# Kernel optimization log

Measured on AMD Instinct MI355X. Metric: run time of the kernel, lower is better.

## Reference

```python
import jax, jax.numpy as jnp
import numpy as np

NUM_GRAPHS = 128
EPS = 1e-5


def _instance_norm(x, seg):
    # per-graph (segment) normalization over rows, per channel; affine=False (PyG default)
    ones = jnp.ones((x.shape[0],), x.dtype)
    cnt = jnp.maximum(jax.ops.segment_sum(ones, seg, num_segments=NUM_GRAPHS), 1.0)[:, None]
    mean = jax.ops.segment_sum(x, seg, num_segments=NUM_GRAPHS) / cnt
    ex2 = jax.ops.segment_sum(x * x, seg, num_segments=NUM_GRAPHS) / cnt
    var = jnp.maximum(ex2 - mean * mean, 0.0)
    return (x - mean[seg]) * jax.lax.rsqrt(var[seg] + EPS)


def setup_inputs() -> dict:
    key = jax.random.key(0)
    ks = jax.random.split(key, 6)
    N, E, H = 100_000, 1_600_000, 64
    emb = jax.random.normal(ks[0], (N, H), jnp.float32)
    edge_index = jax.random.randint(ks[1], (2, E), 0, N)
    batch = jnp.sort(jax.random.randint(ks[2], (N,), 0, NUM_GRAPHS))
    s = lambda fan: 1.0 / np.sqrt(fan)
    # MLP layers [2H, 4H, H, 1]
    W1 = jax.random.uniform(ks[3], (2 * H, 4 * H), jnp.float32, -s(2 * H), s(2 * H))
    b1 = jnp.zeros((4 * H,), jnp.float32)
    W2 = jax.random.uniform(ks[4], (4 * H, H), jnp.float32, -s(4 * H), s(4 * H))
    b2 = jnp.zeros((H,), jnp.float32)
    W3 = jax.random.uniform(ks[5], (H, 1), jnp.float32, -s(H), s(H))
    b3 = jnp.zeros((1,), jnp.float32)
    return dict(emb=emb, edge_index=edge_index, batch=batch,
                W1=W1, b1=b1, W2=W2, b2=b2, W3=W3, b3=b3)


def reference(emb, edge_index, batch, W1, b1, W2, b2, W3, b3):
    col, row = edge_index[0], edge_index[1]
    # edge-wise gather + concat: [E, 2H]
    f12 = jnp.concatenate([emb[col], emb[row]], axis=-1)
    seg = batch[col]  # graph id per edge
    h = jax.nn.relu(_instance_norm(f12 @ W1 + b1, seg))   # [E, 4H]
    h = jax.nn.relu(_instance_norm(h @ W2 + b2, seg))     # [E, H]
    att_log_logits = h @ W3 + b3                          # [E, 1]
    return att_log_logits
```

## Files before the change

kernel.cpp:

```cpp
#include <hip/hip_runtime.h>
#include <hip/hip_bf16.h>

#define NSEG 128
#define H64 64
#define C1 256
#define K1 128
#define C2 64
#define EPSV 1e-5f
#define NWG 256

typedef __attribute__((ext_vector_type(8))) short bf16x8;
typedef __attribute__((ext_vector_type(16))) float f32x16;
typedef __attribute__((ext_vector_type(4))) unsigned int u32x4;

struct BTrue  { static constexpr bool value = true; };
struct BFalse { static constexpr bool value = false; };

__device__ __forceinline__ unsigned short f2bf(float f){
  unsigned int x = __float_as_uint(f);
  x += 0x7fffu + ((x >> 16) & 1u);
  return (unsigned short)(x >> 16);
}
__device__ __forceinline__ float bf2f(unsigned short u){
  return __uint_as_float(((unsigned int)u) << 16);
}
__device__ __forceinline__ unsigned pkbf(float lo, float hi){
  unsigned r;
  asm("v_cvt_pk_bf16_f32 %0, %1, %2" : "=v"(r) : "v"(lo), "v"(hi));
  return r;
}
__device__ __forceinline__ bf16x8 mk8(unsigned a, unsigned b, unsigned c, unsigned d){
  u32x4 t = {a, b, c, d};
  return __builtin_bit_cast(bf16x8, t);
}
__device__ __forceinline__ int xcd_swz(int bid, int nwg){
  int q = nwg >> 3, r = nwg & 7;
  int x = bid & 7, o = bid >> 3;
  return (x < r ? x * (q + 1) : r * (q + 1) + (x - r) * q) + o;
}

__global__ void k_cvt_emb(const float* __restrict__ src, unsigned short* __restrict__ dst, int n4){
  int i = blockIdx.x * blockDim.x + threadIdx.x;
  if (i >= n4) return;
  float4 v = ((const float4*)src)[i];
  unsigned int a = (unsigned int)f2bf(v.x) | ((unsigned int)f2bf(v.y) << 16);
  unsigned int b = (unsigned int)f2bf(v.z) | ((unsigned int)f2bf(v.w) << 16);
  ((uint2*)dst)[i] = make_uint2(a, b);
}

__global__ void k_cvt_w(const float* __restrict__ W1, const float* __restrict__ W2,
                        unsigned short* __restrict__ W1T, unsigned short* __restrict__ W2T){
  int i = blockIdx.x * blockDim.x + threadIdx.x;
  if (i < C1 * K1){
    int c = i >> 7, k = i & 127;
    W1T[i] = f2bf(W1[k * C1 + c]);
  } else {
    int j = i - C1 * K1;
    if (j < C2 * C1){
      int c = j >> 8, k = j & 255;
      W2T[j] = f2bf(W2[k * C2 + c]);
    }
  }
}

__global__ void k_hist(const int* __restrict__ col, const int* __restrict__ batch,
                       int* __restrict__ segE, int* __restrict__ cnt, int E){
  __shared__ int h[NSEG];
  for (int i = threadIdx.x; i < NSEG; i += blockDim.x) h[i] = 0;
  __syncthreads();
  int stride = gridDim.x * blockDim.x;
  for (int e = blockIdx.x * blockDim.x + threadIdx.x; e < E; e += stride){
    int s = batch[col[e]];
    segE[e] = s;
    atomicAdd(&h[s], 1);
  }
  __syncthreads();
  for (int i = threadIdx.x; i < NSEG; i += blockDim.x)
    if (h[i]) atomicAdd(&cnt[i], h[i]);
}

__global__ void k_scan(const int* __restrict__ cnt, int* __restrict__ cursor,
                       float* __restrict__ cntf){
  if (threadIdx.x == 0){
    int acc = 0;
    for (int i = 0; i < NSEG; i++){ cursor[i] = acc; acc += cnt[i]; }
  }
  if (threadIdx.x < NSEG){
    int c = cnt[threadIdx.x];
    cntf[threadIdx.x] = (float)(c > 0 ? c : 1);
  }
}

__global__ void k_scatter(const int* __restrict__ segE, const int* __restrict__ ei,
                          int* __restrict__ cursor, int* __restrict__ perm,
                          int* __restrict__ segS, int* __restrict__ ecol, int* __restrict__ erow,
                          int E, int epb){
  __shared__ int h[NSEG];
  __shared__ int base[NSEG];
  int b0 = blockIdx.x * epb;
  int b1 = b0 + epb < E ? b0 + epb : E;
  for (int i = threadIdx.x; i < NSEG; i += blockDim.x) h[i] = 0;
  __syncthreads();
  for (int e = b0 + threadIdx.x; e < b1; e += blockDim.x) atomicAdd(&h[segE[e]], 1);
  __syncthreads();
  for (int i = threadIdx.x; i < NSEG; i += blockDim.x)
    base[i] = h[i] ? atomicAdd(&cursor[i], h[i]) : 0;
  __syncthreads();
  for (int i = threadIdx.x; i < NSEG; i += blockDim.x) h[i] = 0;
  __syncthreads();
  for (int e = b0 + threadIdx.x; e < b1; e += blockDim.x){
    int s = segE[e];
    int p = base[s] + atomicAdd(&h[s], 1);
    perm[p] = e; segS[p] = s;
    ecol[p] = ei[e]; erow[p] = ei[(size_t)E + e];
  }
}

__global__ void __launch_bounds__(1024, 4)
k_stats1(const unsigned short* __restrict__ ebf, const unsigned short* __restrict__ W1T,
         const int* __restrict__ ecol, const int* __restrict__ erow, const int* __restrict__ segS,
         float* __restrict__ sum1, float* __restrict__ sq1, int NWT, int E, int T)
{
  __shared__ __align__(16) char wl[65536];
  {
    #pragma unroll
    for (int j = 0; j < 4; j++){
      int i = threadIdx.x + j * 1024;
      int r = i >> 4, u = i & 15;
      u32x4 v = *(const u32x4*)(W1T + (size_t)r * K1 + u * 8);
      *(u32x4*)(wl + r * 256 + ((u ^ (r & 15)) << 4)) = v;
    }
  }
  __syncthreads();

  const int lane = threadIdx.x & 63, w = threadIdx.x >> 6;
  const int g = lane >> 5, l31 = lane & 31;
  const int bid = xcd_swz(blockIdx.x, NWG);
  const int wt0 = (bid * 16 + w) * T;
  float psum[8] = {0,0,0,0,0,0,0,0}, psq[8] = {0,0,0,0,0,0,0,0};
  int cur = -1;

  auto flush = [&](int seg){
    if (seg < 0) return;
    #pragma unroll
    for (int nt = 0; nt < 8; nt++){
      float sv = psum[nt] + __shfl_xor(psum[nt], 32);
      float qv = psq[nt]  + __shfl_xor(psq[nt], 32);
      if (lane < 32){
        atomicAdd(&sum1[seg * C1 + nt * 32 + l31], sv);
        atomicAdd(&sq1 [seg * C1 + nt * 32 + l31], qv);
      }
      psum[nt] = 0.f; psq[nt] = 0.f;
    }
  };

  for (int it = 0; it < T; ++it){
    int wt = wt0 + it;
    if (wt >= NWT) break;
    const int p0 = wt * 32;
    int e0 = p0 + l31;
    int e0c = e0 < E ? e0 : E - 1;
    int cA = ecol[e0c], rA = erow[e0c];
    int sg = segS[e0c];

    bf16x8 fa[8];
    #pragma unroll
    for (int kk = 0; kk < 8; kk++){
      int off = (kk & 3) * 16 + g * 8;
      fa[kk] = *(const bf16x8*)(ebf + (size_t)(kk < 4 ? cA : rA) * H64 + off);
    }

    int sA = __builtin_amdgcn_readfirstlane(__shfl(sg, 0));
    int sB = __builtin_amdgcn_readfirstlane(__shfl(sg, 31));
    bool uni = (sA == sB) && (p0 + 32 <= E);
    if (uni && sA != cur){ flush(cur); cur = sA; }
    if (!uni){ flush(cur); cur = -1; }

    #pragma unroll 1
    for (int nt = 0; nt < 8; nt++){
      f32x16 a0;
      #pragma unroll
      for (int r = 0; r < 16; r++) a0[r] = 0.f;
      const int rw = nt * 32 + l31;
      __builtin_amdgcn_s_setprio(1);
      #pragma unroll
      for (int kk = 0; kk < 8; kk++){
        bf16x8 b = *(const bf16x8*)(wl + rw * 256 + (((2 * kk + g) ^ (rw & 15)) << 4));
        a0 = __builtin_amdgcn_mfma_f32_32x32x16_bf16(fa[kk], b, a0, 0, 0, 0);
      }
      __builtin_amdgcn_s_setprio(0);
      if (uni){
        float ts = 0.f, tq = 0.f;
        #pragma unroll
        for (int r = 0; r < 16; r++){ ts += a0[r]; tq += a0[r] * a0[r]; }
        psum[nt] += ts; psq[nt] += tq;
      } else {
        for (int s = sA; s <= sB; s++){
          float ts = 0.f, tq = 0.f;
          #pragma unroll
          for (int r = 0; r < 16; r++){
            int c = (r & 3) + 8 * (r >> 2) + 4 * g;
            bool ok = (__shfl(sg, c) == s) && (p0 + c < E);
            float v = ok ? a0[r] : 0.f;
            ts += v; tq += v * v;
          }
          float sv = ts + __shfl_xor(ts, 32);
          float qv = tq + __shfl_xor(tq, 32);
          if (lane < 32){
            atomicAdd(&sum1[s * C1 + nt * 32 + l31], sv);
            atomicAdd(&sq1 [s * C1 + nt * 32 + l31], qv);
          }
        }
      }
    }
  }
  flush(cur);
}

__global__ void k_fin(const float* __restrict__ sum, const float* __restrict__ sq,
                      const float* __restrict__ cntf,
                      float* __restrict__ sc, float* __restrict__ sh, int C){
  int i = blockIdx.x * blockDim.x + threadIdx.x;
  if (i >= NSEG * C) return;
  int s = i / C;
  float c = cntf[s];
  float m = sum[i] / c;
  float v = fmaxf(sq[i] / c - m * m, 0.f);
  float inv = rsqrtf(v + EPSV);
  sc[i] = inv;
  sh[i] = -m * inv;
}

template<int MODE>
__global__ void __launch_bounds__(1024, 4)
k_mid(const unsigned short* __restrict__ ebf, const unsigned short* __restrict__ W1T,
      const unsigned short* __restrict__ W2T,
      const int* __restrict__ ecol, const int* __restrict__ erow,
      const int* __restrict__ segS, const int* __restrict__ perm,
      const float* __restrict__ sc1, const float* __restrict__ sh1,
      float* __restrict__ sum2, float* __restrict__ sq2,
      unsigned int* __restrict__ y2u,
      const float* __restrict__ sc2, const float* __restrict__ sh2,
      const float* __restrict__ W3, const float* __restrict__ b3,
      float* __restrict__ out, int NWT, int E, int T)
{
  __shared__ __align__(16) char wl[98304];
  {
    #pragma unroll
    for (int j = 0; j < 4; j++){
      int i = threadIdx.x + j * 1024;
      int r = i >> 4, u = i & 15;
      u32x4 v = *(const u32x4*)(W1T + (size_t)r * K1 + u * 8);
      *(u32x4*)(wl + r * 256 + ((u ^ (r & 15)) << 4)) = v;
    }
    #pragma unroll
    for (int j = 0; j < 2; j++){
      int i = threadIdx.x + j * 1024;
      int r = i >> 5, u = i & 31;
      u32x4 v = *(const u32x4*)(W2T + (size_t)r * C1 + u * 8);
      *(u32x4*)(wl + 65536 + r * 512 + ((u ^ (r & 31)) << 4)) = v;
    }
  }
  __syncthreads();

  const int lane = threadIdx.x & 63, w = threadIdx.x >> 6;
  const int g = lane >> 5, l31 = lane & 31;
  const int bid = xcd_swz(blockIdx.x, NWG);
  const int wt0 = (bid * 16 + w) * T;

  float b3v = 0.f;
  if (MODE == 2) b3v = b3[0];

  auto body = [&](auto uni_c, const bf16x8* fbp, int sgn, int sAr, f32x16* acc2){
    constexpr bool UNI = decltype(uni_c)::value;
    #pragma unroll 1
    for (int mt = 0; mt < 8; mt++){
      f32x16 a1;
      #pragma unroll
      for (int r = 0; r < 16; r++) a1[r] = 0.f;
      const int rw = mt * 32 + l31;
      __builtin_amdgcn_s_setprio(1);
      #pragma unroll
      for (int kk = 0; kk < 8; kk++){
        bf16x8 wa = *(const bf16x8*)(wl + rw * 256 + (((2 * kk + g) ^ (rw & 15)) << 4));
        a1 = __builtin_amdgcn_mfma_f32_32x32x16_bf16(wa, fbp[kk], a1, 0, 0, 0);
      }
      __builtin_amdgcn_s_setprio(0);
      const float* scp; const float* shp;
      if constexpr (UNI){
        scp = sc1 + sAr * C1 + mt * 32;
        shp = sh1 + sAr * C1 + mt * 32;
      } else {
        scp = sc1 + sgn * C1 + mt * 32;
        shp = sh1 + sgn * C1 + mt * 32;
      }
      unsigned pk_[8];
      #pragma unroll
      for (int rq = 0; rq < 4; rq++){
        float4 sc = *(const float4*)(scp + rq * 8 + 4 * g);
        float4 sh = *(const float4*)(shp + rq * 8 + 4 * g);
        float h0 = fmaxf(fmaf(a1[rq * 4 + 0], sc.x, sh.x), 0.f);
        float h1 = fmaxf(fmaf(a1[rq * 4 + 1], sc.y, sh.y), 0.f);
        float h2 = fmaxf(fmaf(a1[rq * 4 + 2], sc.z, sh.z), 0.f);
        float h3 = fmaxf(fmaf(a1[rq * 4 + 3], sc.w, sh.w), 0.f);
        pk_[rq * 2 + 0] = pkbf(h0, h1);
        pk_[rq * 2 + 1] = pkbf(h2, h3);
      }
      asm("v_permlane32_swap_b32 %0, %1" : "+v"(pk_[0]), "+v"(pk_[2]));
      asm("v_permlane32_swap_b32 %0, %1" : "+v"(pk_[1]), "+v"(pk_[3]));
      asm("v_permlane32_swap_b32 %0, %1" : "+v"(pk_[4]), "+v"(pk_[6]));
      asm("v_permlane32_swap_b32 %0, %1" : "+v"(pk_[5]), "+v"(pk_[7]));
      bf16x8 bf0 = mk8(pk_[0], pk_[1], pk_[2], pk_[3]);
      bf16x8 bf1 = mk8(pk_[4], pk_[5], pk_[6], pk_[7]);
      __builtin_amdgcn_s_setprio(1);
      #pragma unroll
      for (int ct = 0; ct < 2; ct++){
        int rb = ct * 32 + l31;
        bf16x8 wb0 = *(const bf16x8*)(wl + 65536 + rb * 512 + (((4 * mt + g) ^ (rb & 31)) << 4));
        bf16x8 wb1 = *(const bf16x8*)(wl + 65536 + rb * 512 + (((4 * mt + 2 + g) ^ (rb & 31)) << 4));
        acc2[ct] = __builtin_amdgcn_mfma_f32_32x32x16_bf16(wb0, bf0, acc2[ct], 0, 0, 0);
        acc2[ct] = __builtin_amdgcn_mfma_f32_32x32x16_bf16(wb1, bf1, acc2[ct], 0, 0, 0);
      }
      __builtin_amdgcn_s_setprio(0);
    }
  };

  for (int it = 0; it < T; ++it){
    int wt = wt0 + it;
    if (wt >= NWT) break;
    const int p0 = wt * 32;
    int e0 = p0 + l31;
    bool v0 = e0 < E;
    int e0c = v0 ? e0 : E - 1;
    int cA = ecol[e0c], rA = erow[e0c];
    int sg = segS[e0c];

    bf16x8 fb[8];
    #pragma unroll
    for (int kk = 0; kk < 8; kk++){
      int off = (kk & 3) * 16 + g * 8;
      fb[kk] = *(const bf16x8*)(ebf + (size_t)(kk < 4 ? cA : rA) * H64 + off);
    }

    int sA = __builtin_amdgcn_readfirstlane(__shfl(sg, 0));
    int sB = __builtin_amdgcn_readfirstlane(__shfl(sg, 31));
    const bool uni = (sA == sB) && (p0 + 32 <= E);

    f32x16 acc2[2];
    #pragma unroll
    for (int ct = 0; ct < 2; ct++)
      #pragma unroll
      for (int r = 0; r < 16; r++) acc2[ct][r] = 0.f;

    if (uni) body(BTrue{},  fb, sg, sA, acc2);
    else     body(BFalse{}, fb, sg, sA, acc2);

    if constexpr (MODE == 0){
      if (v0){
        unsigned* yp = y2u + (size_t)e0 * 32;
        #pragma unroll
        for (int ct = 0; ct < 2; ct++)
          #pragma unroll
          for (int rq = 0; rq < 4; rq++){
            uint2 pv;
            pv.x = pkbf(acc2[ct][rq * 4 + 0], acc2[ct][rq * 4 + 1]);
            pv.y = pkbf(acc2[ct][rq * 4 + 2], acc2[ct][rq * 4 + 3]);
            *(uint2*)(yp + ct * 16 + rq * 4 + 2 * g) = pv;
          }
      }
    } else if constexpr (MODE == 1){
      for (int s = sA; s <= sB; s++){
        #pragma unroll
        for (int ct = 0; ct < 2; ct++)
          #pragma unroll
          for (int r = 0; r < 16; r++){
            float x = (v0 && sg == s) ? acc2[ct][r] : 0.f;
            float vs = x, vq = x * x;
            #pragma unroll
            for (int off = 1; off < 32; off <<= 1){
              vs += __shfl_xor(vs, off);
              vq += __shfl_xor(vq, off);
            }
            if (l31 == 0){
              int c2 = ct * 32 + (r & 3) + 8 * (r >> 2) + 4 * g;
              atomicAdd(&sum2[s * C2 + c2], vs);
              atomicAdd(&sq2 [s * C2 + c2], vq);
            }
          }
      }
    } else {
      float acc = 0.f;
      #pragma unroll
      for (int ct = 0; ct < 2; ct++)
        #pragma unroll
        for (int rq = 0; rq < 4; rq++){
          float4 sc = *(const float4*)(sc2 + sg * C2 + ct * 32 + rq * 8 + 4 * g);
          float4 sh = *(const float4*)(sh2 + sg * C2 + ct * 32 + rq * 8 + 4 * g);
          float4 wq = *(const float4*)(W3 + ct * 32 + rq * 8 + 4 * g);
          acc = fmaf(fmaxf(fmaf(acc2[ct][rq * 4 + 0], sc.x, sh.x), 0.f), wq.x, acc);
          acc = fmaf(fmaxf(fmaf(acc2[ct][rq * 4 + 1], sc.y, sh.y), 0.f), wq.y, acc);
          acc = fmaf(fmaxf(fmaf(acc2[ct][rq * 4 + 2], sc.z, sh.z), 0.f), wq.z, acc);
          acc = fmaf(fmaxf(fmaf(acc2[ct][rq * 4 + 3], sc.w, sh.w), 0.f), wq.w, acc);
        }
      acc += __shfl_xor(acc, 32);
      if (g == 0 && v0) out[perm[e0]] = acc + b3v;
    }
  }
}

__global__ void k_stats2(const unsigned int* __restrict__ y2u, const int* __restrict__ segS,
                         float* __restrict__ sum2, float* __restrict__ sq2, int E)
{
  const int cp = threadIdx.x & 31;
  const int es = threadIdx.x >> 5;
  int chunk = (E + gridDim.x - 1) / gridDim.x;
  int eb = blockIdx.x * chunk;
  int ee = eb + chunk < E ? eb + chunk : E;
  float s0 = 0.f, s1 = 0.f, q0 = 0.f, q1 = 0.f;
  int cur = -1;
  for (int e = eb + es; e < ee; e += 8){
    int sg = segS[e];
    unsigned v = y2u[(size_t)e * 32 + cp];
    float f0 = bf2f((unsigned short)(v & 0xffff));
    float f1 = bf2f((unsigned short)(v >> 16));
    if (sg != cur){
      if (cur >= 0){
        atomicAdd(&sum2[cur * C2 + 2 * cp], s0);
        atomicAdd(&sum2[cur * C2 + 2 * cp + 1], s1);
        atomicAdd(&sq2 [cur * C2 + 2 * cp], q0);
        atomicAdd(&sq2 [cur * C2 + 2 * cp + 1], q1);
      }
      s0 = s1 = q0 = q1 = 0.f; cur = sg;
    }
    s0 += f0; s1 += f1; q0 += f0 * f0; q1 += f1 * f1;
  }
  if (cur >= 0){
    atomicAdd(&sum2[cur * C2 + 2 * cp], s0);
    atomicAdd(&sum2[cur * C2 + 2 * cp + 1], s1);
    atomicAdd(&sq2 [cur * C2 + 2 * cp], q0);
    atomicAdd(&sq2 [cur * C2 + 2 * cp + 1], q1);
  }
}

__global__ void k_out(const unsigned short* __restrict__ y2, const int* __restrict__ segS,
                      const int* __restrict__ perm, const float* __restrict__ sc2,
                      const float* __restrict__ sh2, const float* __restrict__ W3,
                      const float* __restrict__ b3, float* __restrict__ out, int E)
{
  const int lane = threadIdx.x & 63;
  const int wid = (blockIdx.x * blockDim.x + threadIdx.x) >> 6;
  const int nw = (gridDim.x * blockDim.x) >> 6;
  const int es = lane >> 3;
  const int cp = (lane & 7) * 8;
  float w3r[8];
  #pragma unroll
  for (int j = 0; j < 8; j++) w3r[j] = W3[cp + j];
  const float b3v = b3[0];
  for (long base = (long)wid * 8; base < E; base += (long)nw * 8){
    int pos = (int)base + es;
    float a = 0.f;
    if (pos < E){
      bf16x8 v = *(const bf16x8*)(y2 + (size_t)pos * C2 + cp);
      int s = segS[pos];
      const float* scp = sc2 + s * C2 + cp;
      const float* shp = sh2 + s * C2 + cp;
      #pragma unroll
      for (int j = 0; j < 8; j++){
        float hv = fmaxf(fmaf(bf2f((unsigned short)v[j]), scp[j], shp[j]), 0.f);
        a = fmaf(hv, w3r[j], a);
      }
    }
    a += __shfl_xor(a, 1); a += __shfl_xor(a, 2); a += __shfl_xor(a, 4);
    if ((lane & 7) == 0 && pos < E) out[perm[pos]] = a + b3v;
  }
}

extern "C" void kernel_launch(void* const* d_in, const int* in_sizes, int n_in,
                              void* d_out, int out_size, void* d_ws, size_t ws_size,
                              hipStream_t stream)
{
  const float* emb   = (const float*)d_in[0];
  const int*   ei    = (const int*)d_in[1];
  const int*   batch = (const int*)d_in[2];
  const float* W1    = (const float*)d_in[3];
  const float* W2    = (const float*)d_in[5];
  const float* W3    = (const float*)d_in[7];
  const float* b3    = (const float*)d_in[8];
  float* out = (float*)d_out;
  const int E = in_sizes[1] / 2;
  const int N = in_sizes[0] / H64;
  const int NWT = (E + 31) / 32;

  char* ws = (char*)d_ws;
  size_t o = 0;
  auto al = [&](size_t b){ size_t r = o; o = (o + b + 255) & ~((size_t)255); return r; };
  size_t o_ebf  = al((size_t)N * H64 * 2);
  size_t o_w1t  = al((size_t)C1 * K1 * 2);
  size_t o_w2t  = al((size_t)C2 * C1 * 2);
  size_t o_perm = al((size_t)E * 4);
  size_t o_segS = al((size_t)E * 4);
  size_t o_ecol = al((size_t)E * 4);
  size_t o_erow = al((size_t)E * 4);
  size_t o_cnt  = al(NSEG * 4);
  size_t o_cur  = al(NSEG * 4);
  size_t o_cntf = al(NSEG * 4);
  size_t o_sum1 = al((size_t)NSEG * C1 * 4);
  size_t o_sq1  = al((size_t)NSEG * C1 * 4);
  size_t o_sum2 = al((size_t)NSEG * C2 * 4);
  size_t o_sq2  = al((size_t)NSEG * C2 * 4);
  size_t o_sc1  = al((size_t)NSEG * C1 * 4);
  size_t o_sh1  = al((size_t)NSEG * C1 * 4);
  size_t o_sc2  = al((size_t)NSEG * C2 * 4);
  size_t o_sh2  = al((size_t)NSEG * C2 * 4);
  size_t o_segE = al((size_t)E * 4);
  size_t o_y2   = o_segE;
  size_t need_full = o_segE + (size_t)E * C2 * 2;
  const bool full = ws_size >= need_full;

  unsigned short* ebf = (unsigned short*)(ws + o_ebf);
  unsigned short* W1T = (unsigned short*)(ws + o_w1t);
  unsigned short* W2T = (unsigned short*)(ws + o_w2t);
  int* perm = (int*)(ws + o_perm);
  int* segS = (int*)(ws + o_segS);
  int* ecol = (int*)(ws + o_ecol);
  int* erow = (int*)(ws + o_erow);
  int* cnt  = (int*)(ws + o_cnt);
  int* curp = (int*)(ws + o_cur);
  float* cntf = (float*)(ws + o_cntf);
  float* sum1 = (float*)(ws + o_sum1);
  float* sq1  = (float*)(ws + o_sq1);
  float* sum2 = (float*)(ws + o_sum2);
  float* sq2  = (float*)(ws + o_sq2);
  float* sc1  = (float*)(ws + o_sc1);
  float* sh1  = (float*)(ws + o_sh1);
  float* sc2  = (float*)(ws + o_sc2);
  float* sh2  = (float*)(ws + o_sh2);
  int* segE = (int*)(ws + o_segE);
  unsigned int* y2u = (unsigned int*)(ws + o_y2);
  unsigned short* y2 = (unsigned short*)(ws + o_y2);

  hipMemsetAsync(ws + o_cnt, 0, o_sc1 - o_cnt, stream);

  k_cvt_emb<<<(N * H64 / 4 + 255) / 256, 256, 0, stream>>>(emb, ebf, N * H64 / 4);
  k_cvt_w<<<192, 256, 0, stream>>>(W1, W2, W1T, W2T);

  k_hist<<<2048, 256, 0, stream>>>(ei, batch, segE, cnt, E);
  k_scan<<<1, 128, 0, stream>>>(cnt, curp, cntf);
  const int epb = 2048;
  k_scatter<<<(E + epb - 1) / epb, 256, 0, stream>>>(segE, ei, curp, perm, segS, ecol, erow, E, epb);

  const int T = (NWT + NWG * 16 - 1) / (NWG * 16);
  k_stats1<<<NWG, 1024, 0, stream>>>(ebf, W1T, ecol, erow, segS, sum1, sq1, NWT, E, T);
  k_fin<<<(NSEG * C1) / 256, 256, 0, stream>>>(sum1, sq1, cntf, sc1, sh1, C1);

  if (full){
    k_mid<0><<<NWG, 1024, 0, stream>>>(ebf, W1T, W2T, ecol, erow, segS, perm,
        sc1, sh1, sum2, sq2, y2u, sc2, sh2, W3, b3, out, NWT, E, T);
    k_stats2<<<512, 256, 0, stream>>>(y2u, segS, sum2, sq2, E);
    k_fin<<<(NSEG * C2) / 256, 256, 0, stream>>>(sum2, sq2, cntf, sc2, sh2, C2);
    k_out<<<1024, 256, 0, stream>>>(y2, segS, perm, sc2, sh2, W3, b3, out, E);
  } else {
    k_mid<1><<<NWG, 1024, 0, stream>>>(ebf, W1T, W2T, ecol, erow, segS, perm,
        sc1, sh1, sum2, sq2, nullptr, sc2, sh2, W3, b3, out, NWT, E, T);
    k_fin<<<(NSEG * C2) / 256, 256, 0, stream>>>(sum2, sq2, cntf, sc2, sh2, C2);
    k_mid<2><<<NWG, 1024, 0, stream>>>(ebf, W1T, W2T, ecol, erow, segS, perm,
        sc1, sh1, sum2, sq2, nullptr, sc2, sh2, W3, b3, out, NWT, E, T);
  }
}
```

Baseline: 700.9 us.

## Prefetch next tile indices, pair MFMA tiles, cache norm params in LDS

Edge indices and segment ids for the next 32-edge tile are loaded one iteration ahead, so their latency is hidden behind the current tile's MFMA work. In the stats1 kernel two output column tiles are now computed per loop iteration, which gives the MFMA pipe two independent accumulator chains. In k_mid the per-segment scale and shift vectors are staged into a per-wave LDS slot when the segment changes, replacing repeated global reads on the uniform path. The cost is extra registers, which could lower occupancy under the 1024x4 launch bounds, plus another 32KB of shared memory on top of 96KB that may limit the number of resident blocks.

```diff
diff --git a/kernel.cpp b/kernel.cpp
--- a/kernel.cpp
+++ b/kernel.cpp
@@ -154,14 +154,22 @@
     }
   };
 
+  auto ld3 = [&](int wt, int& a, int& r, int& s){
+    int e = wt * 32 + l31;
+    int ec = e < E ? e : E - 1;
+    a = ecol[ec]; r = erow[ec]; s = segS[ec];
+  };
+
+  int cA, rA, sg;
+  if (wt0 < NWT) ld3(wt0, cA, rA, sg);
+
   for (int it = 0; it < T; ++it){
     int wt = wt0 + it;
     if (wt >= NWT) break;
     const int p0 = wt * 32;
-    int e0 = p0 + l31;
-    int e0c = e0 < E ? e0 : E - 1;
-    int cA = ecol[e0c], rA = erow[e0c];
-    int sg = segS[e0c];
+    int nA, nR, nS;
+    const bool hv = (it + 1 < T) && (wt + 1 < NWT);
+    if (hv) ld3(wt + 1, nA, nR, nS);
 
     bf16x8 fa[8];
     #pragma unroll
@@ -177,42 +185,56 @@
     if (!uni){ flush(cur); cur = -1; }
 
     #pragma unroll 1
-    for (int nt = 0; nt < 8; nt++){
-      f32x16 a0;
-      #pragma unroll
-      for (int r = 0; r < 16; r++) a0[r] = 0.f;
-      const int rw = nt * 32 + l31;
+    for (int np = 0; np < 4; np++){
+      const int nt0 = 2 * np, nt1 = 2 * np + 1;
+      f32x16 a0, a1;
+      #pragma unroll
+      for (int r = 0; r < 16; r++){ a0[r] = 0.f; a1[r] = 0.f; }
+      const int rw0 = nt0 * 32 + l31, rw1 = nt1 * 32 + l31;
       __builtin_amdgcn_s_setprio(1);
       #pragma unroll
       for (int kk = 0; kk < 8; kk++){
-        bf16x8 b = *(const bf16x8*)(wl + rw * 256 + (((2 * kk + g) ^ (rw & 15)) << 4));
-        a0 = __builtin_amdgcn_mfma_f32_32x32x16_bf16(fa[kk], b, a0, 0, 0, 0);
+        bf16x8 b0 = *(const bf16x8*)(wl + rw0 * 256 + (((2 * kk + g) ^ (rw0 & 15)) << 4));
+        bf16x8 b1 = *(const bf16x8*)(wl + rw1 * 256 + (((2 * kk + g) ^ (rw1 & 15)) << 4));
+        a0 = __builtin_amdgcn_mfma_f32_32x32x16_bf16(fa[kk], b0, a0, 0, 0, 0);
+        a1 = __builtin_amdgcn_mfma_f32_32x32x16_bf16(fa[kk], b1, a1, 0, 0, 0);
       }
       __builtin_amdgcn_s_setprio(0);
       if (uni){
-        float ts = 0.f, tq = 0.f;
+        float t0 = 0.f, q0 = 0.f, t1 = 0.f, q1 = 0.f;
         #pragma unroll
-        for (int r = 0; r < 16; r++){ ts += a0[r]; tq += a0[r] * a0[r]; }
-        psum[nt] += ts; psq[nt] += tq;
+        for (int r = 0; r < 16; r++){
+          t0 += a0[r]; q0 += a0[r] * a0[r];
+          t1 += a1[r]; q1 += a1[r] * a1[r];
+        }
+        psum[nt0] += t0; psq[nt0] += q0;
+        psum[nt1] += t1; psq[nt1] += q1;
       } else {
         for (int s = sA; s <= sB; s++){
-          float ts = 0.f, tq = 0.f;
+          float t0 = 0.f, q0 = 0.f, t1 = 0.f, q1 = 0.f;
           #pragma unroll
           for (int r = 0; r < 16; r++){
             int c = (r & 3) + 8 * (r >> 2) + 4 * g;
             bool ok = (__shfl(sg, c) == s) && (p0 + c < E);
-            float v = ok ? a0[r] : 0.f;
-            ts += v; tq += v * v;
+            float v0 = ok ? a0[r] : 0.f;
+            float v1 = ok ? a1[r] : 0.f;
+            t0 += v0; q0 += v0 * v0;
+            t1 += v1; q1 += v1 * v1;
           }
-          float sv = ts + __shfl_xor(ts, 32);
-          float qv = tq + __shfl_xor(tq, 32);
+          float s0 = t0 + __shfl_xor(t0, 32);
+          float qq0 = q0 + __shfl_xor(q0, 32);
+          float s1 = t1 + __shfl_xor(t1, 32);
+          float qq1 = q1 + __shfl_xor(q1, 32);
           if (lane < 32){
-            atomicAdd(&sum1[s * C1 + nt * 32 + l31], sv);
-            atomicAdd(&sq1 [s * C1 + nt * 32 + l31], qv);
+            atomicAdd(&sum1[s * C1 + nt0 * 32 + l31], s0);
+            atomicAdd(&sq1 [s * C1 + nt0 * 32 + l31], qq0);
+            atomicAdd(&sum1[s * C1 + nt1 * 32 + l31], s1);
+            atomicAdd(&sq1 [s * C1 + nt1 * 32 + l31], qq1);
           }
         }
       }
     }
+    if (hv){ cA = nA; rA = nR; sg = nS; }
   }
   flush(cur);
 }
@@ -245,6 +267,7 @@
       float* __restrict__ out, int NWT, int E, int T)
 {
   __shared__ __align__(16) char wl[98304];
+  __shared__ __align__(16) float scsh[16][512];
   {
     #pragma unroll
     for (int j = 0; j < 4; j++){
@@ -270,8 +293,9 @@
 
   float b3v = 0.f;
   if (MODE == 2) b3v = b3[0];
-
-  auto body = [&](auto uni_c, const bf16x8* fbp, int sgn, int sAr, f32x16* acc2){
+  int wseg = -1;
+
+  auto body = [&](auto uni_c, const bf16x8* fbp, int sgn, f32x16* acc2){
     constexpr bool UNI = decltype(uni_c)::value;
     #pragma unroll 1
     for (int mt = 0; mt < 8; mt++){
@@ -286,19 +310,17 @@
         a1 = __builtin_amdgcn_mfma_f32_32x32x16_bf16(wa, fbp[kk], a1, 0, 0, 0);
       }
       __builtin_amdgcn_s_setprio(0);
-      const float* scp; const float* shp;
-      if constexpr (UNI){
-        scp = sc1 + sAr * C1 + mt * 32;
-        shp = sh1 + sAr * C1 + mt * 32;
-      } else {
-        scp = sc1 + sgn * C1 + mt * 32;
-        shp = sh1 + sgn * C1 + mt * 32;
-      }
       unsigned pk_[8];
       #pragma unroll
       for (int rq = 0; rq < 4; rq++){
-        float4 sc = *(const float4*)(scp + rq * 8 + 4 * g);
-        float4 sh = *(const float4*)(shp + rq * 8 + 4 * g);
+        float4 sc, sh;
+        if constexpr (UNI){
+          sc = *(const float4*)(&scsh[w][mt * 32 + rq * 8 + 4 * g]);
+          sh = *(const float4*)(&scsh[w][256 + mt * 32 + rq * 8 + 4 * g]);
+        } else {
+          sc = *(const float4*)(sc1 + sgn * C1 + mt * 32 + rq * 8 + 4 * g);
+          sh = *(const float4*)(sh1 + sgn * C1 + mt * 32 + rq * 8 + 4 * g);
+        }
         float h0 = fmaxf(fmaf(a1[rq * 4 + 0], sc.x, sh.x), 0.f);
         float h1 = fmaxf(fmaf(a1[rq * 4 + 1], sc.y, sh.y), 0.f);
         float h2 = fmaxf(fmaf(a1[rq * 4 + 2], sc.z, sh.z), 0.f);
@@ -325,15 +347,25 @@
     }
   };
 
+  auto ld3 = [&](int wt, int& a, int& r, int& s){
+    int e = wt * 32 + l31;
+    int ec = e < E ? e : E - 1;
+    a = ecol[ec]; r = erow[ec]; s = segS[ec];
+  };
+
+  int cA, rA, sg;
+  if (wt0 < NWT) ld3(wt0, cA, rA, sg);
+
   for (int it = 0; it < T; ++it){
     int wt = wt0 + it;
     if (wt >= NWT) break;
     const int p0 = wt * 32;
+    int nA, nR, nS;
+    const bool hv = (it + 1 < T) && (wt + 1 < NWT);
+    if (hv) ld3(wt + 1, nA, nR, nS);
+
     int e0 = p0 + l31;
     bool v0 = e0 < E;
-    int e0c = v0 ? e0 : E - 1;
-    int cA = ecol[e0c], rA = erow[e0c];
-    int sg = segS[e0c];
 
     bf16x8 fb[8];
     #pragma unroll
@@ -346,14 +378,22 @@
     int sB = __builtin_amdgcn_readfirstlane(__shfl(sg, 31));
     const bool uni = (sA == sB) && (p0 + 32 <= E);
 
+    if (uni && sA != wseg){
+      float4 s4 = *(const float4*)(sc1 + sA * C1 + lane * 4);
+      float4 h4 = *(const float4*)(sh1 + sA * C1 + lane * 4);
+      *(float4*)(&scsh[w][lane * 4]) = s4;
+      *(float4*)(&scsh[w][256 + lane * 4]) = h4;
+      wseg = sA;
+    }
+
     f32x16 acc2[2];
     #pragma unroll
     for (int ct = 0; ct < 2; ct++)
       #pragma unroll
       for (int r = 0; r < 16; r++) acc2[ct][r] = 0.f;
 
-    if (uni) body(BTrue{},  fb, sg, sA, acc2);
-    else     body(BFalse{}, fb, sg, sA, acc2);
+    if (uni) body(BTrue{},  fb, sg, acc2);
+    else     body(BFalse{}, fb, sg, acc2);
 
     if constexpr (MODE == 0){
       if (v0){
@@ -405,6 +445,7 @@
       acc += __shfl_xor(acc, 32);
       if (g == 0 && v0) out[perm[e0]] = acc + b3v;
     }
+    if (hv){ cA = nA; rA = nR; sg = nS; }
   }
 }
 
```

Result: faster. 674.1 us (-3.8%).
